# Optimization experiments

Hardware: AMD Instinct MI355X
Metric: run time of the kernel (lower is better)

Reference implementation:

```python
import jax, jax.numpy as jnp
import numpy as np

B, S, IN, H, SS = 128, 128, 2, 512, 100


def _gru_cell(x, h, Wi, Wh, bi, bh):
    # PyTorch GRU gate order: r, z, n
    gi = x @ Wi.T + bi
    gh = h @ Wh.T + bh
    ir, iz, inn = jnp.split(gi, 3, axis=-1)
    hr, hz, hn = jnp.split(gh, 3, axis=-1)
    r = jax.nn.sigmoid(ir + hr)
    z = jax.nn.sigmoid(iz + hz)
    n = jnp.tanh(inn + r * hn)
    return (1.0 - z) * n + z * h


def setup_inputs() -> dict:
    key = jax.random.key(0)
    ks = jax.random.split(key, 20)
    s = 1.0 / np.sqrt(H)
    inp = {
        "instance": jax.random.normal(ks[0], (B, S, IN), jnp.float32),
        "solution": jax.random.randint(ks[1], (B, S), 0, S),
        "instance_hidden": jax.random.normal(ks[2], (B, S, H), jnp.float32),
        "eps": jax.random.normal(ks[3], (B, SS), jnp.float32),
        # reference_embedding: Linear(IN -> H)
        "Wr": jax.random.normal(ks[4], (H, IN), jnp.float32) * s,
        "br": jnp.zeros((H,), jnp.float32),
        # rnn: GRU(H, H)
        "Wi1": jax.random.normal(ks[5], (3 * H, H), jnp.float32) * s,
        "Wh1": jax.random.normal(ks[6], (3 * H, H), jnp.float32) * s,
        "bi1": jnp.zeros((3 * H,), jnp.float32),
        "bh1": jnp.zeros((3 * H,), jnp.float32),
        # encoder_attn (additive)
        "Wa": jax.random.normal(ks[7], (H, H), jnp.float32) * s,
        "Ua": jax.random.normal(ks[8], (H, H), jnp.float32) * s,
        "v": jax.random.normal(ks[9], (H,), jnp.float32) * s,
        # gru_decoder: GRU(2H, H)
        "Wi2": jax.random.normal(ks[10], (3 * H, 2 * H), jnp.float32) * s,
        "Wh2": jax.random.normal(ks[11], (3 * H, H), jnp.float32) * s,
        "bi2": jnp.zeros((3 * H,), jnp.float32),
        "bh2": jnp.zeros((3 * H,), jnp.float32),
        # fc1 / fc2: Linear(H -> SS)
        "W1": jax.random.normal(ks[12], (SS, H), jnp.float32) * s,
        "b1": jnp.zeros((SS,), jnp.float32),
        "W2": jax.random.normal(ks[13], (SS, H), jnp.float32) * s,
        "b2": jnp.zeros((SS,), jnp.float32),
    }
    return inp


def reference(instance, solution, instance_hidden, eps, Wr, br, Wi1, Wh1, bi1, bh1,
              Wa, Ua, v, Wi2, Wh2, bi2, bh2, W1, b1, W2, b2):
    # gather reference nodes for every step, embed once: (B, L, H)
    inst_sel = jnp.take_along_axis(instance, solution[:, :, None], axis=1)  # (B,L,IN)
    ref_emb = inst_sel @ Wr.T + br                                          # (B,L,H)

    # precompute attention projection of the (static) instance encoding
    inst_proj = jnp.einsum("bsh,kh->bsk", instance_hidden, Wa)              # (B,S,H)

    L = solution.shape[1]
    x1_seq = jnp.swapaxes(ref_emb[:, : L - 1], 0, 1)  # (L-1,B,H) input to rnn (node j-1)
    x2_seq = jnp.swapaxes(ref_emb[:, 1:], 0, 1)       # (L-1,B,H) ref embed of node j

    def step(carry, xs):
        h1, h2 = carry
        x1, x2ref = xs
        h1 = _gru_cell(x1, h1, Wi1, Wh1, bi1, bh1)
        scores = jnp.einsum("bsh,h->bs", jnp.tanh(inst_proj + (h1 @ Ua.T)[:, None, :]), v)
        attn = jax.nn.softmax(scores, axis=-1)                 # (B,S)
        context = jnp.einsum("bs,bsh->bh", attn, instance_hidden)
        h2 = _gru_cell(jnp.concatenate([x2ref, context], axis=-1), h2, Wi2, Wh2, bi2, bh2)
        return (h1, h2), None

    h0 = jnp.zeros((instance.shape[0], Wh1.shape[1]), instance.dtype)
    (_, h2), _ = jax.lax.scan(step, (h0, h0), (x1_seq, x2_seq))

    mu = h2 @ W1.T + b1
    log_var = h2 @ W2.T + b2
    z = mu + eps * jnp.exp(0.5 * log_var)
    return z, mu, log_var
```

## Files before the change

kernel.cpp:

```cpp
#include <hip/hip_runtime.h>
#include <math.h>


__device__ __forceinline__ float sigm(float x){ return 1.0f/(1.0f+__expf(-x)); }
__device__ __forceinline__ float tanh_(float x){ float e=__expf(2.0f*x); return 1.0f-2.0f/(e+1.0f); }

__global__ __launch_bounds__(256)
void prep_kernel(const float* __restrict__ instance, const int* __restrict__ solution,
                 const float* __restrict__ Hst, const float* __restrict__ Wr,
                 const float* __restrict__ br, const float* __restrict__ Wi1,
                 const float* __restrict__ bi1, const float* __restrict__ Wh1,
                 const float* __restrict__ Wa, const float* __restrict__ Ua,
                 const float* __restrict__ Wi2, const float* __restrict__ Wh2,
                 const float* __restrict__ bi2,
                 float* __restrict__ P, float* __restrict__ WhT1, float* __restrict__ UaT,
                 float* __restrict__ WD, float* __restrict__ xselT,
                 float* __restrict__ A1f, float* __restrict__ A2f,
                 float* __restrict__ c1f, float* __restrict__ c2f,
                 float* __restrict__ h1T, float* __restrict__ vstack)
{
  const int w = blockIdx.x, t = threadIdx.x;
  __shared__ float smem[6656];

  if (w < 1024) {
    const int m0 = (w >> 3) * 128, h0 = (w & 7) * 64;
    const int hl = t & 15, mseg = t >> 4;
    float acc[4][8];
#pragma unroll
    for (int i = 0; i < 4; ++i)
#pragma unroll
      for (int r = 0; r < 8; ++r) acc[i][r] = 0.f;
    for (int kt = 0; kt < 16; ++kt) {
      {
        int row = t >> 1, cb = (t & 1) * 16;
        const float4* sp = (const float4*)(Hst + (size_t)(m0 + row) * 512 + kt * 32 + cb);
        float4 q0 = sp[0], q1 = sp[1], q2 = sp[2], q3 = sp[3];
        float vals[16] = {q0.x,q0.y,q0.z,q0.w,q1.x,q1.y,q1.z,q1.w,
                          q2.x,q2.y,q2.z,q2.w,q3.x,q3.y,q3.z,q3.w};
#pragma unroll
        for (int i = 0; i < 16; ++i) smem[(cb + i) * 136 + row] = vals[i];
      }
      {
        int row = t >> 2, cb = (t & 3) * 8;
        const float4* sp = (const float4*)(Wa + (size_t)(h0 + row) * 512 + kt * 32 + cb);
        float4 q0 = sp[0], q1 = sp[1];
        float vals[8] = {q0.x,q0.y,q0.z,q0.w,q1.x,q1.y,q1.z,q1.w};
#pragma unroll
        for (int i = 0; i < 8; ++i) smem[4352 + (cb + i) * 72 + row] = vals[i];
      }
      __syncthreads();
#pragma unroll 8
      for (int kk = 0; kk < 32; ++kk) {
        float4 wv = *(const float4*)&smem[4352 + kk * 72 + hl * 4];
        float4 ha = *(const float4*)&smem[kk * 136 + mseg * 8];
        float4 hb = *(const float4*)&smem[kk * 136 + mseg * 8 + 4];
        float wv_[4] = {wv.x, wv.y, wv.z, wv.w};
        float hv_[8] = {ha.x, ha.y, ha.z, ha.w, hb.x, hb.y, hb.z, hb.w};
#pragma unroll
        for (int i = 0; i < 4; ++i)
#pragma unroll
          for (int r = 0; r < 8; ++r) acc[i][r] += wv_[i] * hv_[r];
      }
      __syncthreads();
    }
#pragma unroll
    for (int r = 0; r < 8; ++r) {
      float4 st = {acc[0][r], acc[1][r], acc[2][r], acc[3][r]};
      *(float4*)&P[(size_t)(m0 + mseg * 8 + r) * 512 + h0 + hl * 4] = st;
    }

  } else if (w < 1664) {
    const int wt = w - 1024;
    const float* sp; float* dp; int r0, c0; size_t srs, drs;
    if (wt < 192)      { int q = wt;       sp = Wh1;       dp = WhT1;           r0=(q/8)*64; c0=(q%8)*64; srs=512;  drs=1536; }
    else if (wt < 384) { int q = wt - 192; sp = Wh2;       dp = WD;             r0=(q/8)*64; c0=(q%8)*64; srs=512;  drs=1536; }
    else if (wt < 576) { int q = wt - 384; sp = Wi2 + 512; dp = WD + 512*1536;  r0=(q/8)*64; c0=(q%8)*64; srs=1024; drs=1536; }
    else               { int q = wt - 576; sp = Ua;        dp = UaT;            r0=(q/8)*64; c0=(q%8)*64; srs=512;  drs=512;  }
    int row = t >> 2, cb = (t & 3) * 16;
    const float4* s2 = (const float4*)(sp + (size_t)(r0 + row) * srs + c0 + cb);
    float4 q0 = s2[0], q1 = s2[1], q2 = s2[2], q3 = s2[3];
    float vals[16] = {q0.x,q0.y,q0.z,q0.w,q1.x,q1.y,q1.z,q1.w,
                      q2.x,q2.y,q2.z,q2.w,q3.x,q3.y,q3.z,q3.w};
#pragma unroll
    for (int i = 0; i < 16; ++i) smem[row * 65 + cb + i] = vals[i];
    __syncthreads();
    float* d2 = dp + (size_t)(c0 + row) * drs + r0 + cb;
#pragma unroll
    for (int g = 0; g < 4; ++g) {
      float4 o = {smem[(cb + g*4 + 0) * 65 + row], smem[(cb + g*4 + 1) * 65 + row],
                  smem[(cb + g*4 + 2) * 65 + row], smem[(cb + g*4 + 3) * 65 + row]};
      *(float4*)(d2 + g * 4) = o;
    }

  } else if (w < 2048) {
    const int wf = w - 1664, wv = t >> 6, lane = t & 63;
    const int j = wf * 4 + wv;
    const float4* w1p = (const float4*)(Wi1 + (size_t)j * 512 + lane * 8);
    const float4* w2p = (const float4*)(Wi2 + (size_t)j * 1024 + lane * 8);
    const float4* wrp = (const float4*)(Wr + lane * 16);
    const float4* brp = (const float4*)(br + lane * 8);
    float4 u0 = w1p[0], u1 = w1p[1], v0 = w2p[0], v1 = w2p[1];
    float4 r0 = wrp[0], r1 = wrp[1], r2 = wrp[2], r3 = wrp[3];
    float4 bb0 = brp[0], bb1 = brp[1];
    float w1a[8] = {u0.x,u0.y,u0.z,u0.w,u1.x,u1.y,u1.z,u1.w};
    float w2a[8] = {v0.x,v0.y,v0.z,v0.w,v1.x,v1.y,v1.z,v1.w};
    float wr0[8] = {r0.x,r0.z,r1.x,r1.z,r2.x,r2.z,r3.x,r3.z};
    float wr1[8] = {r0.y,r0.w,r1.y,r1.w,r2.y,r2.w,r3.y,r3.w};
    float bra[8] = {bb0.x,bb0.y,bb0.z,bb0.w,bb1.x,bb1.y,bb1.z,bb1.w};
    float a0=0,a1=0,cc=0,b0=0,b1=0,cc2=0;
#pragma unroll
    for (int i = 0; i < 8; ++i) {
      a0 += w1a[i]*wr0[i]; a1 += w1a[i]*wr1[i]; cc  += w1a[i]*bra[i];
      b0 += w2a[i]*wr0[i]; b1 += w2a[i]*wr1[i]; cc2 += w2a[i]*bra[i];
    }
#pragma unroll
    for (int off = 32; off; off >>= 1) {
      a0 += __shfl_xor(a0, off); a1 += __shfl_xor(a1, off); cc  += __shfl_xor(cc, off);
      b0 += __shfl_xor(b0, off); b1 += __shfl_xor(b1, off); cc2 += __shfl_xor(cc2, off);
    }
    if (lane == 0) {
      A1f[j*2] = a0; A1f[j*2+1] = a1; c1f[j] = cc + bi1[j];
      A2f[j*2] = b0; A2f[j*2+1] = b1; c2f[j] = cc2 + bi2[j];
    }

  } else if (w == 2048) {
    for (int o = t; o < 32768; o += 256) {
      int b = o & 127, r = o >> 7, d = r & 1, l = r >> 1;
      int sel = solution[b * 128 + l];
      xselT[o] = instance[(size_t)(b * 128 + sel) * 2 + d];
    }
  } else {
    const int wz = w - 2049;
    for (int i = 0; i < 32; ++i) {
      int idx = wz * 8192 + i * 256 + t;
      h1T[65536 + idx] = 0.f;
      vstack[idx] = 0.f;
    }
  }
}

__global__ __launch_bounds__(512)
void step_kernel(int k, const float* __restrict__ Hst, const float* __restrict__ bh1,
                 const float* __restrict__ vvec, const float* __restrict__ bh2,
                 const float* __restrict__ P, const float* __restrict__ WhT1,
                 const float* __restrict__ UaT, const float* __restrict__ WD,
                 const float* __restrict__ xselT, const float* __restrict__ A1f,
                 const float* __restrict__ A2f, const float* __restrict__ c1f,
                 const float* __restrict__ c2f,
                 float* __restrict__ h1T, float* __restrict__ vstack,
                 float* __restrict__ uT, float* __restrict__ part,
                 float* __restrict__ mzbuf)
{
  const int w = blockIdx.x, t = threadIdx.x;
  __shared__ float lds[6144];

  if (w < 256) {
    const int tA = k; if (tA > 126) return;
    const int wv = __builtin_amdgcn_readfirstlane(t >> 6);
    const int lane = t & 63;
    const int c0 = w * 2;
    const float* h1p = h1T + ((tA + 1) & 1) * 65536;
    float acc[12];
#pragma unroll
    for (int i = 0; i < 12; ++i) acc[i] = 0.f;
    const float* hrow = h1p + wv * 64 * 128 + lane * 2;
    const float* wrow = WhT1 + (size_t)(wv * 64) * 1536 + c0;
    for (int kk = 0; kk < 64; ++kk) {
      float2 hv = *(const float2*)hrow;
      float w00 = wrow[0],    w01 = wrow[1];
      float w10 = wrow[512],  w11 = wrow[513];
      float w20 = wrow[1024], w21 = wrow[1025];
      acc[0] += hv.x*w00; acc[1] += hv.y*w00; acc[2]  += hv.x*w01; acc[3]  += hv.y*w01;
      acc[4] += hv.x*w10; acc[5] += hv.y*w10; acc[6]  += hv.x*w11; acc[7]  += hv.y*w11;
      acc[8] += hv.x*w20; acc[9] += hv.y*w20; acc[10] += hv.x*w21; acc[11] += hv.y*w21;
      hrow += 128; wrow += 1536;
    }
#pragma unroll
    for (int i = 0; i < 12; ++i) lds[(wv * 12 + i) * 64 + lane] = acc[i];
    __syncthreads();
    if (t < 256) {
      int b = t & 127, ci = t >> 7, ln = b >> 1, bs = b & 1;
      float gr = 0, gz = 0, gn = 0;
#pragma unroll
      for (int w2 = 0; w2 < 8; ++w2) {
        gr += lds[(w2 * 12 +     ci * 2 + bs) * 64 + ln];
        gz += lds[(w2 * 12 + 4 + ci * 2 + bs) * 64 + ln];
        gn += lds[(w2 * 12 + 8 + ci * 2 + bs) * 64 + ln];
      }
      int c = c0 + ci;
      float x0 = xselT[(tA * 2) * 128 + b], x1 = xselT[(tA * 2 + 1) * 128 + b];
      float ir  = A1f[c*2]*x0          + A1f[c*2+1]*x1          + c1f[c];
      float iz  = A1f[(c+512)*2]*x0    + A1f[(c+512)*2+1]*x1    + c1f[c+512];
      float in_ = A1f[(c+1024)*2]*x0   + A1f[(c+1024)*2+1]*x1   + c1f[c+1024];
      float r = sigm(ir + gr + bh1[c]);
      float z = sigm(iz + gz + bh1[c + 512]);
      float n = tanh_(in_ + r * (gn + bh1[c + 1024]));
      float hp = h1p[c * 128 + b];
      h1T[(tA & 1) * 65536 + c * 128 + b] = (1.f - z) * n + z * hp;
    }

  } else if (w < 384) {
    const int tU = k - 1; if (tU < 0 || tU > 126) return;
    const int wv = __builtin_amdgcn_readfirstlane(t >> 6);
    const int lane = t & 63;
    const int c0 = (w - 256) * 4;
    const float* h1c = h1T + (tU & 1) * 65536;
    float acc[8];
#pragma unroll
    for (int i = 0; i < 8; ++i) acc[i] = 0.f;
    const float* hrow = h1c + wv * 64 * 128 + lane * 2;
    const float* wrow = UaT + (size_t)(wv * 64) * 512 + c0;
    for (int kk = 0; kk < 64; ++kk) {
      float2 hv = *(const float2*)hrow;
      float w0 = wrow[0], w1 = wrow[1], w2 = wrow[2], w3 = wrow[3];
      acc[0] += hv.x*w0; acc[1] += hv.y*w0; acc[2] += hv.x*w1; acc[3] += hv.y*w1;
      acc[4] += hv.x*w2; acc[5] += hv.y*w2; acc[6] += hv.x*w3; acc[7] += hv.y*w3;
      hrow += 128; wrow += 512;
    }
#pragma unroll
    for (int i = 0; i < 8; ++i) lds[(wv * 8 + i) * 64 + lane] = acc[i];
    __syncthreads();
    {
      int b = t & 127, q = t >> 7;
      float u = 0;
#pragma unroll
      for (int w2 = 0; w2 < 8; ++w2) u += lds[(w2 * 8 + q * 2 + (b & 1)) * 64 + (b >> 1)];
      uT[(tU & 1) * 65536 + (c0 + q) * 128 + b] = u;
    }

  } else if (w < 896) {
    const int tB = k - 2; if (tB < 0 || tB > 126) return;
    const int wb = w - 384, b = wb >> 2, q = wb & 3;
    const int slot = tB & 1;
    float* uS = lds, *vS = lds + 512, *scS = lds + 1024, *wgt = lds + 1056;
    uS[t] = uT[slot * 65536 + t * 128 + b];
    vS[t] = vvec[t];
    __syncthreads();
    const int wv8 = t >> 6, lane = t & 63, h0 = lane * 8;
#pragma unroll
    for (int si = 0; si < 4; ++si) {
      int s = q * 32 + wv8 * 4 + si;
      const float* prow = P + (size_t)(b * 128 + s) * 512 + h0;
      float4 p0 = ((const float4*)prow)[0];
      float4 p1 = ((const float4*)prow)[1];
      float val = tanh_(p0.x + uS[h0+0]) * vS[h0+0]
                + tanh_(p0.y + uS[h0+1]) * vS[h0+1]
                + tanh_(p0.z + uS[h0+2]) * vS[h0+2]
                + tanh_(p0.w + uS[h0+3]) * vS[h0+3]
                + tanh_(p1.x + uS[h0+4]) * vS[h0+4]
                + tanh_(p1.y + uS[h0+5]) * vS[h0+5]
                + tanh_(p1.z + uS[h0+6]) * vS[h0+6]
                + tanh_(p1.w + uS[h0+7]) * vS[h0+7];
#pragma unroll
      for (int off = 32; off; off >>= 1) val += __shfl_xor(val, off);
      if (lane == 0) scS[wv8 * 4 + si] = val;
    }
    __syncthreads();
    if (t < 32) {
      float sc = scS[t], m = sc;
#pragma unroll
      for (int off = 16; off; off >>= 1) m = fmaxf(m, __shfl_xor(m, off));
      float e = __expf(sc - m);
      float zz = e;
#pragma unroll
      for (int off = 16; off; off >>= 1) zz += __shfl_xor(zz, off);
      wgt[t] = e;
      if (t == 0) {
        int mzi = ((slot * 4 + q) * 128 + b) * 2;
        mzbuf[mzi] = m; mzbuf[mzi + 1] = zz;
      }
    }
    __syncthreads();
    float a = 0.f;
    const float* hb = Hst + (size_t)(b * 128 + q * 32) * 512 + t;
#pragma unroll 8
    for (int s = 0; s < 32; ++s) a += wgt[s] * hb[(size_t)s * 512];
    part[((size_t)(slot * 4 + q) * 128 + b) * 512 + t] = a;

  } else if (w < 928) {
    const int tC = k - 3; if (tC < 0 || tC > 126) return;
    const int slot = tC & 1;
    float* scale = lds;
    if (t < 128) {
      int b = t;
      float m0 = mzbuf[((slot*4+0)*128+b)*2], z0 = mzbuf[((slot*4+0)*128+b)*2+1];
      float m1 = mzbuf[((slot*4+1)*128+b)*2], z1 = mzbuf[((slot*4+1)*128+b)*2+1];
      float m2 = mzbuf[((slot*4+2)*128+b)*2], z2 = mzbuf[((slot*4+2)*128+b)*2+1];
      float m3 = mzbuf[((slot*4+3)*128+b)*2], z3 = mzbuf[((slot*4+3)*128+b)*2+1];
      float M = fmaxf(fmaxf(m0, m1), fmaxf(m2, m3));
      float e0 = __expf(m0 - M), e1 = __expf(m1 - M), e2 = __expf(m2 - M), e3 = __expf(m3 - M);
      float inv = 1.f / (z0*e0 + z1*e1 + z2*e2 + z3*e3);
      scale[b] = e0*inv; scale[128+b] = e1*inv; scale[256+b] = e2*inv; scale[384+b] = e3*inv;
    }
    __syncthreads();
    const int base = (w - 896) * 2048;
#pragma unroll
    for (int i = 0; i < 4; ++i) {
      int o = base + i * 512 + t;
      int b = o & 127, kk = o >> 7;
      float vsum = scale[b]       * part[((size_t)(slot*4+0)*128 + b)*512 + kk]
                 + scale[128 + b] * part[((size_t)(slot*4+1)*128 + b)*512 + kk]
                 + scale[256 + b] * part[((size_t)(slot*4+2)*128 + b)*512 + kk]
                 + scale[384 + b] * part[((size_t)(slot*4+3)*128 + b)*512 + kk];
      vstack[slot * 131072 + (512 + kk) * 128 + b] = vsum;
    }

  } else {
    const int tD = k - 4; if (tD < 0 || tD > 126) return;
    const int wv = __builtin_amdgcn_readfirstlane(t >> 6);
    const int lane = t & 63;
    const int c0 = (w - 928) * 2;
    const int pair = tD & 1;
    const float* vs = vstack + pair * 131072;
    float acc[12];
#pragma unroll
    for (int i = 0; i < 12; ++i) acc[i] = 0.f;
    const float* hrow = vs + wv * 128 * 128 + lane * 2;
    const float* wrow = WD + (size_t)(wv * 128) * 1536 + c0;
    for (int kk = 0; kk < 128; ++kk) {
      float2 hv = *(const float2*)hrow;
      float w00 = wrow[0],    w01 = wrow[1];
      float w10 = wrow[512],  w11 = wrow[513];
      float w20 = wrow[1024], w21 = wrow[1025];
      acc[0] += hv.x*w00; acc[1] += hv.y*w00; acc[2]  += hv.x*w01; acc[3]  += hv.y*w01;
      acc[4] += hv.x*w10; acc[5] += hv.y*w10; acc[6]  += hv.x*w11; acc[7]  += hv.y*w11;
      acc[8] += hv.x*w20; acc[9] += hv.y*w20; acc[10] += hv.x*w21; acc[11] += hv.y*w21;
      hrow += 128; wrow += 1536;
    }
#pragma unroll
    for (int i = 0; i < 12; ++i) lds[(wv * 12 + i) * 64 + lane] = acc[i];
    __syncthreads();
    if (t < 256) {
      int b = t & 127, ci = t >> 7, ln = b >> 1, bs = b & 1;
      float gr = 0, gz = 0, gnh = 0, gni = 0;
#pragma unroll
      for (int w2 = 0; w2 < 8; ++w2) {
        gr += lds[(w2 * 12 +     ci * 2 + bs) * 64 + ln];
        gz += lds[(w2 * 12 + 4 + ci * 2 + bs) * 64 + ln];
        float g = lds[(w2 * 12 + 8 + ci * 2 + bs) * 64 + ln];
        if (w2 < 4) gnh += g; else gni += g;
      }
      int c = c0 + ci;
      float x0 = xselT[((tD + 1) * 2) * 128 + b], x1 = xselT[((tD + 1) * 2 + 1) * 128 + b];
      float ir  = A2f[c*2]*x0        + A2f[c*2+1]*x1        + c2f[c];
      float iz  = A2f[(c+512)*2]*x0  + A2f[(c+512)*2+1]*x1  + c2f[c+512];
      float in_ = A2f[(c+1024)*2]*x0 + A2f[(c+1024)*2+1]*x1 + c2f[c+1024] + gni;
      float r = sigm(ir + gr + bh2[c]);
      float z = sigm(iz + gz + bh2[c + 512]);
      float n = tanh_(in_ + r * (gnh + bh2[c + 1024]));
      float hp = vs[c * 128 + b];
      vstack[((tD + 1) & 1) * 131072 + c * 128 + b] = (1.f - z) * n + z * hp;
    }
  }
}

__global__ __launch_bounds__(128)
void final_kernel(const float* __restrict__ vstack, const float* __restrict__ eps,
                  const float* __restrict__ W1, const float* __restrict__ b1,
                  const float* __restrict__ W2, const float* __restrict__ b2,
                  float* __restrict__ out)
{
  const int b = blockIdx.x, t = threadIdx.x;
  __shared__ float hS[512];
  const float* h2 = vstack + 131072;
  for (int i = t; i < 512; i += 128) hS[i] = h2[i * 128 + b];
  __syncthreads();
  if (t < 100) {
    const float* w1 = W1 + (size_t)t * 512;
    const float* w2 = W2 + (size_t)t * 512;
    float mu = b1[t], lv = b2[t];
    for (int kk = 0; kk < 512; ++kk) { float h = hS[kk]; mu += h * w1[kk]; lv += h * w2[kk]; }
    float zz = mu + eps[b * 100 + t] * __expf(0.5f * lv);
    out[b * 100 + t] = zz;
    out[12800 + b * 100 + t] = mu;
    out[25600 + b * 100 + t] = lv;
  }
}

extern "C" void kernel_launch(void* const* d_in, const int* in_sizes, int n_in,
                              void* d_out, int out_size, void* d_ws, size_t ws_size,
                              hipStream_t stream)
{
  const float* instance = (const float*)d_in[0];
  const int*   solution = (const int*)d_in[1];
  const float* Hst      = (const float*)d_in[2];
  const float* eps      = (const float*)d_in[3];
  const float* Wr  = (const float*)d_in[4];
  const float* br  = (const float*)d_in[5];
  const float* Wi1 = (const float*)d_in[6];
  const float* Wh1 = (const float*)d_in[7];
  const float* bi1 = (const float*)d_in[8];
  const float* bh1 = (const float*)d_in[9];
  const float* Wa  = (const float*)d_in[10];
  const float* Ua  = (const float*)d_in[11];
  const float* v   = (const float*)d_in[12];
  const float* Wi2 = (const float*)d_in[13];
  const float* Wh2 = (const float*)d_in[14];
  const float* bi2 = (const float*)d_in[15];
  const float* bh2 = (const float*)d_in[16];
  const float* W1  = (const float*)d_in[17];
  const float* b1  = (const float*)d_in[18];
  const float* W2  = (const float*)d_in[19];
  const float* b2  = (const float*)d_in[20];

  float* wsf   = (float*)d_ws;
  float* P     = wsf;
  float* WhT1  = P     + 8388608;
  float* UaT   = WhT1  + 786432;
  float* WD    = UaT   + 262144;
  float* xselT = WD    + 1572864;
  float* A1f   = xselT + 32768;
  float* A2f   = A1f   + 3072;
  float* c1f   = A2f   + 3072;
  float* c2f   = c1f   + 1536;
  float* h1T   = c2f   + 1536;
  float* vstack= h1T   + 131072;
  float* uT    = vstack+ 262144;
  float* part  = uT    + 131072;
  float* mzbuf = part  + 524288;

  prep_kernel<<<dim3(2057), dim3(256), 0, stream>>>(
      instance, solution, Hst, Wr, br, Wi1, bi1, Wh1, Wa, Ua, Wi2, Wh2, bi2,
      P, WhT1, UaT, WD, xselT, A1f, A2f, c1f, c2f, h1T, vstack);

  for (int k = 0; k < 131; ++k)
    step_kernel<<<dim3(1184), dim3(512), 0, stream>>>(
        k, Hst, bh1, v, bh2, P, WhT1, UaT, WD, xselT, A1f, A2f, c1f, c2f,
        h1T, vstack, uT, part, mzbuf);

  final_kernel<<<dim3(128), dim3(128), 0, stream>>>(vstack, eps, W1, b1, W2, b2, (float*)d_out);
}
```

Before: 9.455 ms.

## Run GRU-attention recurrence in a persistent cooperative kernel with grid sync

```diff
diff --git a/kernel.cpp b/kernel.cpp
--- a/kernel.cpp
+++ b/kernel.cpp
@@ -1,5 +1,8 @@
 #include <hip/hip_runtime.h>
+#include <hip/hip_cooperative_groups.h>
 #include <math.h>
+
+namespace cg = cooperative_groups;
 
 
 __device__ __forceinline__ float sigm(float x){ return 1.0f/(1.0f+__expf(-x)); }
@@ -13,8 +16,8 @@
                  const float* __restrict__ Wa, const float* __restrict__ Ua,
                  const float* __restrict__ Wi2, const float* __restrict__ Wh2,
                  const float* __restrict__ bi2,
-                 float* __restrict__ P, float* __restrict__ WhT1, float* __restrict__ UaT,
-                 float* __restrict__ WD, float* __restrict__ xselT,
+                 float* __restrict__ P, float* __restrict__ WAs, float* __restrict__ WUs,
+                 float* __restrict__ WDs, float* __restrict__ xselT,
                  float* __restrict__ A1f, float* __restrict__ A2f,
                  float* __restrict__ c1f, float* __restrict__ c2f,
                  float* __restrict__ h1T, float* __restrict__ vstack)
@@ -31,23 +34,19 @@
 #pragma unroll
       for (int r = 0; r < 8; ++r) acc[i][r] = 0.f;
     for (int kt = 0; kt < 16; ++kt) {
-      {
-        int row = t >> 1, cb = (t & 1) * 16;
+      { int row = t >> 1, cb = (t & 1) * 16;
         const float4* sp = (const float4*)(Hst + (size_t)(m0 + row) * 512 + kt * 32 + cb);
         float4 q0 = sp[0], q1 = sp[1], q2 = sp[2], q3 = sp[3];
         float vals[16] = {q0.x,q0.y,q0.z,q0.w,q1.x,q1.y,q1.z,q1.w,
                           q2.x,q2.y,q2.z,q2.w,q3.x,q3.y,q3.z,q3.w};
 #pragma unroll
-        for (int i = 0; i < 16; ++i) smem[(cb + i) * 136 + row] = vals[i];
-      }
-      {
-        int row = t >> 2, cb = (t & 3) * 8;
+        for (int i = 0; i < 16; ++i) smem[(cb + i) * 136 + row] = vals[i]; }
+      { int row = t >> 2, cb = (t & 3) * 8;
         const float4* sp = (const float4*)(Wa + (size_t)(h0 + row) * 512 + kt * 32 + cb);
         float4 q0 = sp[0], q1 = sp[1];
         float vals[8] = {q0.x,q0.y,q0.z,q0.w,q1.x,q1.y,q1.z,q1.w};
 #pragma unroll
-        for (int i = 0; i < 8; ++i) smem[4352 + (cb + i) * 72 + row] = vals[i];
-      }
+        for (int i = 0; i < 8; ++i) smem[4352 + (cb + i) * 72 + row] = vals[i]; }
       __syncthreads();
 #pragma unroll 8
       for (int kk = 0; kk < 32; ++kk) {
@@ -69,29 +68,31 @@
       *(float4*)&P[(size_t)(m0 + mseg * 8 + r) * 512 + h0 + hl * 4] = st;
     }
 
+  } else if (w < 1216) {
+    for (int i = 0; i < 16; ++i) {
+      int e = (w - 1024) * 4096 + i * 256 + t;
+      int fc = e >> 9, k = e & 511;
+      int g = fc >> 9, c = fc & 511;
+      int wg = c >> 1, j = g * 2 + (c & 1);
+      WAs[((size_t)wg * 512 + k) * 8 + j] = Wh1[(size_t)fc * 512 + k];
+    }
+  } else if (w < 1280) {
+    for (int i = 0; i < 16; ++i) {
+      int e = (w - 1216) * 4096 + i * 256 + t;
+      int c = e >> 9, k = e & 511;
+      int wg = c >> 2, j = c & 3;
+      WUs[((size_t)wg * 512 + k) * 4 + j] = Ua[(size_t)c * 512 + k];
+    }
   } else if (w < 1664) {
-    const int wt = w - 1024;
-    const float* sp; float* dp; int r0, c0; size_t srs, drs;
-    if (wt < 192)      { int q = wt;       sp = Wh1;       dp = WhT1;           r0=(q/8)*64; c0=(q%8)*64; srs=512;  drs=1536; }
-    else if (wt < 384) { int q = wt - 192; sp = Wh2;       dp = WD;             r0=(q/8)*64; c0=(q%8)*64; srs=512;  drs=1536; }
-    else if (wt < 576) { int q = wt - 384; sp = Wi2 + 512; dp = WD + 512*1536;  r0=(q/8)*64; c0=(q%8)*64; srs=1024; drs=1536; }
-    else               { int q = wt - 576; sp = Ua;        dp = UaT;            r0=(q/8)*64; c0=(q%8)*64; srs=512;  drs=512;  }
-    int row = t >> 2, cb = (t & 3) * 16;
-    const float4* s2 = (const float4*)(sp + (size_t)(r0 + row) * srs + c0 + cb);
-    float4 q0 = s2[0], q1 = s2[1], q2 = s2[2], q3 = s2[3];
-    float vals[16] = {q0.x,q0.y,q0.z,q0.w,q1.x,q1.y,q1.z,q1.w,
-                      q2.x,q2.y,q2.z,q2.w,q3.x,q3.y,q3.z,q3.w};
-#pragma unroll
-    for (int i = 0; i < 16; ++i) smem[row * 65 + cb + i] = vals[i];
-    __syncthreads();
-    float* d2 = dp + (size_t)(c0 + row) * drs + r0 + cb;
-#pragma unroll
-    for (int g = 0; g < 4; ++g) {
-      float4 o = {smem[(cb + g*4 + 0) * 65 + row], smem[(cb + g*4 + 1) * 65 + row],
-                  smem[(cb + g*4 + 2) * 65 + row], smem[(cb + g*4 + 3) * 65 + row]};
-      *(float4*)(d2 + g * 4) = o;
-    }
-
+    for (int i = 0; i < 16; ++i) {
+      int e = (w - 1280) * 4096 + i * 256 + t;
+      int fc = e >> 10, k = e & 1023;
+      int g = fc >> 9, c = fc & 511;
+      int wg = c >> 1, j = g * 2 + (c & 1);
+      float src = (k < 512) ? Wh2[(size_t)fc * 512 + k]
+                            : Wi2[(size_t)fc * 1024 + 512 + (k - 512)];
+      WDs[((size_t)wg * 1024 + k) * 8 + j] = src;
+    }
   } else if (w < 2048) {
     const int wf = w - 1664, wv = t >> 6, lane = t & 63;
     const int j = wf * 4 + wv;
@@ -122,7 +123,6 @@
       A1f[j*2] = a0; A1f[j*2+1] = a1; c1f[j] = cc + bi1[j];
       A2f[j*2] = b0; A2f[j*2+1] = b1; c2f[j] = cc2 + bi2[j];
     }
-
   } else if (w == 2048) {
     for (int o = t; o < 32768; o += 256) {
       int b = o & 127, r = o >> 7, d = r & 1, l = r >> 1;
@@ -139,219 +139,242 @@
   }
 }
 
-__global__ __launch_bounds__(512)
-void step_kernel(int k, const float* __restrict__ Hst, const float* __restrict__ bh1,
-                 const float* __restrict__ vvec, const float* __restrict__ bh2,
-                 const float* __restrict__ P, const float* __restrict__ WhT1,
-                 const float* __restrict__ UaT, const float* __restrict__ WD,
-                 const float* __restrict__ xselT, const float* __restrict__ A1f,
-                 const float* __restrict__ A2f, const float* __restrict__ c1f,
-                 const float* __restrict__ c2f,
-                 float* __restrict__ h1T, float* __restrict__ vstack,
-                 float* __restrict__ uT, float* __restrict__ part,
-                 float* __restrict__ mzbuf)
-{
+__device__ __forceinline__ void round_body(
+    int k, int w, int t, int wv, int lane, float* lds,
+    const float* __restrict__ Hst, const float* __restrict__ bh1,
+    const float* __restrict__ vvec, const float* __restrict__ bh2,
+    const float* __restrict__ P, const float* __restrict__ WAs,
+    const float* __restrict__ WUs, const float* __restrict__ WDs,
+    const float* __restrict__ xselT, const float* __restrict__ A1f,
+    const float* __restrict__ A2f, const float* __restrict__ c1f,
+    const float* __restrict__ c2f,
+    float* __restrict__ h1T, float* __restrict__ vstack, float* __restrict__ uT)
+{
+  if (w < 256) {
+    const int tA = k;
+    if (tA <= 126) {
+      const int slotW = tA & 1, slotR = slotW ^ 1;
+      const float* hp = h1T + slotR * 65536 + (wv * 128) * 128 + lane * 2;
+      const float4* wp = (const float4*)(WAs + ((size_t)w * 512 + wv * 128) * 8);
+      float acc[12];
+#pragma unroll
+      for (int i = 0; i < 12; ++i) acc[i] = 0.f;
+#pragma unroll 4
+      for (int kk = 0; kk < 128; ++kk) {
+        float2 hv = *(const float2*)(hp + kk * 128);
+        float4 wa = wp[kk * 2], wb = wp[kk * 2 + 1];
+        acc[0] += hv.x*wa.x; acc[1]  += hv.y*wa.x;
+        acc[2] += hv.x*wa.y; acc[3]  += hv.y*wa.y;
+        acc[4] += hv.x*wa.z; acc[5]  += hv.y*wa.z;
+        acc[6] += hv.x*wa.w; acc[7]  += hv.y*wa.w;
+        acc[8] += hv.x*wb.x; acc[9]  += hv.y*wb.x;
+        acc[10]+= hv.x*wb.y; acc[11] += hv.y*wb.y;
+      }
+#pragma unroll
+      for (int i = 0; i < 12; ++i) lds[wv * 768 + i * 64 + lane] = acc[i];
+      __syncthreads();
+      { int b = t & 127, ci = t >> 7, l = b >> 1, bs = b & 1;
+        float gr = 0, gz = 0, gn = 0;
+#pragma unroll
+        for (int w2 = 0; w2 < 4; ++w2) {
+          gr += lds[w2 * 768 + (    ci * 2 + bs) * 64 + l];
+          gz += lds[w2 * 768 + (4 + ci * 2 + bs) * 64 + l];
+          gn += lds[w2 * 768 + (8 + ci * 2 + bs) * 64 + l];
+        }
+        int c = w * 2 + ci;
+        float x0 = xselT[(tA * 2) * 128 + b], x1 = xselT[(tA * 2 + 1) * 128 + b];
+        float ir  = A1f[c*2]*x0        + A1f[c*2+1]*x1        + c1f[c];
+        float iz  = A1f[(c+512)*2]*x0  + A1f[(c+512)*2+1]*x1  + c1f[c+512];
+        float in_ = A1f[(c+1024)*2]*x0 + A1f[(c+1024)*2+1]*x1 + c1f[c+1024];
+        float r = sigm(ir + gr + bh1[c]);
+        float z = sigm(iz + gz + bh1[c + 512]);
+        float n = tanh_(in_ + r * (gn + bh1[c + 1024]));
+        float hpv = h1T[slotR * 65536 + c * 128 + b];
+        h1T[slotW * 65536 + c * 128 + b] = (1.f - z) * n + z * hpv;
+      }
+      __syncthreads();
+    }
+  } else if (w < 384) {
+    const int tU = k - 1;
+    if (tU >= 0 && tU <= 126) {
+      const int slot = tU & 1;
+      const float* hp = h1T + slot * 65536 + (wv * 128) * 128 + lane * 2;
+      const float4* wp = (const float4*)(WUs + ((size_t)(w - 256) * 512 + wv * 128) * 4);
+      float acc[8];
+#pragma unroll
+      for (int i = 0; i < 8; ++i) acc[i] = 0.f;
+#pragma unroll 4
+      for (int kk = 0; kk < 128; ++kk) {
+        float2 hv = *(const float2*)(hp + kk * 128);
+        float4 wq = wp[kk];
+        acc[0] += hv.x*wq.x; acc[1] += hv.y*wq.x;
+        acc[2] += hv.x*wq.y; acc[3] += hv.y*wq.y;
+        acc[4] += hv.x*wq.z; acc[5] += hv.y*wq.z;
+        acc[6] += hv.x*wq.w; acc[7] += hv.y*wq.w;
+      }
+#pragma unroll
+      for (int i = 0; i < 8; ++i) lds[wv * 512 + i * 64 + lane] = acc[i];
+      __syncthreads();
+      { int b = t & 127, qq = t >> 7, l = b >> 1, bs = b & 1;
+        int c0 = (w - 256) * 4;
+#pragma unroll
+        for (int jj = 0; jj < 2; ++jj) {
+          int j = qq + jj * 2;
+          float u = 0;
+#pragma unroll
+          for (int w2 = 0; w2 < 4; ++w2) u += lds[w2 * 512 + (j * 2 + bs) * 64 + l];
+          uT[slot * 65536 + (c0 + j) * 128 + b] = u;
+        }
+      }
+      __syncthreads();
+    }
+  } else if (w < 512) {
+    const int tB = k - 2;
+    if (tB >= 0 && tB <= 126) {
+      const int b = w - 384, slot = tB & 1;
+      float* uS = lds; float* vS = lds + 512; float* scS = lds + 1024; float* wS = lds + 1152;
+      uS[t]       = uT[slot * 65536 + t * 128 + b];
+      uS[t + 256] = uT[slot * 65536 + (t + 256) * 128 + b];
+      vS[t] = vvec[t]; vS[t + 256] = vvec[t + 256];
+      __syncthreads();
+      const int h0 = lane * 8;
+#pragma unroll 2
+      for (int si = 0; si < 32; ++si) {
+        int s = wv * 32 + si;
+        const float* prow = P + ((size_t)(b * 128 + s)) * 512 + h0;
+        float4 p0 = ((const float4*)prow)[0];
+        float4 p1 = ((const float4*)prow)[1];
+        float val = tanh_(p0.x + uS[h0+0]) * vS[h0+0]
+                  + tanh_(p0.y + uS[h0+1]) * vS[h0+1]
+                  + tanh_(p0.z + uS[h0+2]) * vS[h0+2]
+                  + tanh_(p0.w + uS[h0+3]) * vS[h0+3]
+                  + tanh_(p1.x + uS[h0+4]) * vS[h0+4]
+                  + tanh_(p1.y + uS[h0+5]) * vS[h0+5]
+                  + tanh_(p1.z + uS[h0+6]) * vS[h0+6]
+                  + tanh_(p1.w + uS[h0+7]) * vS[h0+7];
+#pragma unroll
+        for (int off = 32; off; off >>= 1) val += __shfl_xor(val, off);
+        if (lane == 0) scS[s] = val;
+      }
+      __syncthreads();
+      if (t < 64) {
+        float sc0 = scS[t], sc1 = scS[t + 64];
+        float m = fmaxf(sc0, sc1);
+#pragma unroll
+        for (int off = 32; off; off >>= 1) m = fmaxf(m, __shfl_xor(m, off));
+        float e0 = __expf(sc0 - m), e1 = __expf(sc1 - m);
+        float zz = e0 + e1;
+#pragma unroll
+        for (int off = 32; off; off >>= 1) zz += __shfl_xor(zz, off);
+        float inv = 1.f / zz;
+        wS[t] = e0 * inv; wS[t + 64] = e1 * inv;
+      }
+      __syncthreads();
+      { float acc0 = 0.f, acc1 = 0.f;
+        const float* hb = Hst + (size_t)(b * 128) * 512;
+#pragma unroll 8
+        for (int s = 0; s < 128; ++s) {
+          float ws_ = wS[s];
+          acc0 += ws_ * hb[(size_t)s * 512 + t];
+          acc1 += ws_ * hb[(size_t)s * 512 + t + 256];
+        }
+        vstack[slot * 131072 + (512 + t) * 128 + b] = acc0;
+        vstack[slot * 131072 + (512 + t + 256) * 128 + b] = acc1;
+      }
+      __syncthreads();
+    }
+  } else {
+    const int tD = k - 3;
+    if (tD >= 0 && tD <= 126) {
+      const int wd = w - 512, slot = tD & 1, nslot = slot ^ 1;
+      const float* vsp = vstack + slot * 131072;
+      const float* hp = vsp + (wv * 256) * 128 + lane * 2;
+      const float4* wp = (const float4*)(WDs + ((size_t)wd * 1024 + wv * 256) * 8);
+      float acc[12];
+#pragma unroll
+      for (int i = 0; i < 12; ++i) acc[i] = 0.f;
+#pragma unroll 4
+      for (int kk = 0; kk < 256; ++kk) {
+        float2 hv = *(const float2*)(hp + kk * 128);
+        float4 wa = wp[kk * 2], wb = wp[kk * 2 + 1];
+        acc[0] += hv.x*wa.x; acc[1]  += hv.y*wa.x;
+        acc[2] += hv.x*wa.y; acc[3]  += hv.y*wa.y;
+        acc[4] += hv.x*wa.z; acc[5]  += hv.y*wa.z;
+        acc[6] += hv.x*wa.w; acc[7]  += hv.y*wa.w;
+        acc[8] += hv.x*wb.x; acc[9]  += hv.y*wb.x;
+        acc[10]+= hv.x*wb.y; acc[11] += hv.y*wb.y;
+      }
+#pragma unroll
+      for (int i = 0; i < 12; ++i) lds[wv * 768 + i * 64 + lane] = acc[i];
+      __syncthreads();
+      { int b = t & 127, ci = t >> 7, l = b >> 1, bs = b & 1;
+        float gr = 0, gz = 0, gnh = 0, gni = 0;
+#pragma unroll
+        for (int w2 = 0; w2 < 4; ++w2) {
+          gr += lds[w2 * 768 + (    ci * 2 + bs) * 64 + l];
+          gz += lds[w2 * 768 + (4 + ci * 2 + bs) * 64 + l];
+          float g = lds[w2 * 768 + (8 + ci * 2 + bs) * 64 + l];
+          if (w2 < 2) gnh += g; else gni += g;
+        }
+        int c = wd * 2 + ci;
+        float x0 = xselT[((tD + 1) * 2) * 128 + b], x1 = xselT[((tD + 1) * 2 + 1) * 128 + b];
+        float ir  = A2f[c*2]*x0        + A2f[c*2+1]*x1        + c2f[c];
+        float iz  = A2f[(c+512)*2]*x0  + A2f[(c+512)*2+1]*x1  + c2f[c+512];
+        float in_ = A2f[(c+1024)*2]*x0 + A2f[(c+1024)*2+1]*x1 + c2f[c+1024] + gni;
+        float r = sigm(ir + gr + bh2[c]);
+        float z = sigm(iz + gz + bh2[c + 512]);
+        float n = tanh_(in_ + r * (gnh + bh2[c + 1024]));
+        float hpv = vsp[c * 128 + b];
+        vstack[nslot * 131072 + c * 128 + b] = (1.f - z) * n + z * hpv;
+      }
+      __syncthreads();
+    }
+  }
+}
+
+__global__ void __launch_bounds__(256, 3)
+persist_kernel(const float* __restrict__ Hst, const float* __restrict__ bh1,
+               const float* __restrict__ vvec, const float* __restrict__ bh2,
+               const float* __restrict__ P, const float* __restrict__ WAs,
+               const float* __restrict__ WUs, const float* __restrict__ WDs,
+               const float* __restrict__ xselT, const float* __restrict__ A1f,
+               const float* __restrict__ A2f, const float* __restrict__ c1f,
+               const float* __restrict__ c2f,
+               float* __restrict__ h1T, float* __restrict__ vstack,
+               float* __restrict__ uT)
+{
+  cg::grid_group grid = cg::this_grid();
   const int w = blockIdx.x, t = threadIdx.x;
-  __shared__ float lds[6144];
-
-  if (w < 256) {
-    const int tA = k; if (tA > 126) return;
-    const int wv = __builtin_amdgcn_readfirstlane(t >> 6);
-    const int lane = t & 63;
-    const int c0 = w * 2;
-    const float* h1p = h1T + ((tA + 1) & 1) * 65536;
-    float acc[12];
-#pragma unroll
-    for (int i = 0; i < 12; ++i) acc[i] = 0.f;
-    const float* hrow = h1p + wv * 64 * 128 + lane * 2;
-    const float* wrow = WhT1 + (size_t)(wv * 64) * 1536 + c0;
-    for (int kk = 0; kk < 64; ++kk) {
-      float2 hv = *(const float2*)hrow;
-      float w00 = wrow[0],    w01 = wrow[1];
-      float w10 = wrow[512],  w11 = wrow[513];
-      float w20 = wrow[1024], w21 = wrow[1025];
-      acc[0] += hv.x*w00; acc[1] += hv.y*w00; acc[2]  += hv.x*w01; acc[3]  += hv.y*w01;
-      acc[4] += hv.x*w10; acc[5] += hv.y*w10; acc[6]  += hv.x*w11; acc[7]  += hv.y*w11;
-      acc[8] += hv.x*w20; acc[9] += hv.y*w20; acc[10] += hv.x*w21; acc[11] += hv.y*w21;
-      hrow += 128; wrow += 1536;
-    }
-#pragma unroll
-    for (int i = 0; i < 12; ++i) lds[(wv * 12 + i) * 64 + lane] = acc[i];
-    __syncthreads();
-    if (t < 256) {
-      int b = t & 127, ci = t >> 7, ln = b >> 1, bs = b & 1;
-      float gr = 0, gz = 0, gn = 0;
-#pragma unroll
-      for (int w2 = 0; w2 < 8; ++w2) {
-        gr += lds[(w2 * 12 +     ci * 2 + bs) * 64 + ln];
-        gz += lds[(w2 * 12 + 4 + ci * 2 + bs) * 64 + ln];
-        gn += lds[(w2 * 12 + 8 + ci * 2 + bs) * 64 + ln];
-      }
-      int c = c0 + ci;
-      float x0 = xselT[(tA * 2) * 128 + b], x1 = xselT[(tA * 2 + 1) * 128 + b];
-      float ir  = A1f[c*2]*x0          + A1f[c*2+1]*x1          + c1f[c];
-      float iz  = A1f[(c+512)*2]*x0    + A1f[(c+512)*2+1]*x1    + c1f[c+512];
-      float in_ = A1f[(c+1024)*2]*x0   + A1f[(c+1024)*2+1]*x1   + c1f[c+1024];
-      float r = sigm(ir + gr + bh1[c]);
-      float z = sigm(iz + gz + bh1[c + 512]);
-      float n = tanh_(in_ + r * (gn + bh1[c + 1024]));
-      float hp = h1p[c * 128 + b];
-      h1T[(tA & 1) * 65536 + c * 128 + b] = (1.f - z) * n + z * hp;
-    }
-
-  } else if (w < 384) {
-    const int tU = k - 1; if (tU < 0 || tU > 126) return;
-    const int wv = __builtin_amdgcn_readfirstlane(t >> 6);
-    const int lane = t & 63;
-    const int c0 = (w - 256) * 4;
-    const float* h1c = h1T + (tU & 1) * 65536;
-    float acc[8];
-#pragma unroll
-    for (int i = 0; i < 8; ++i) acc[i] = 0.f;
-    const float* hrow = h1c + wv * 64 * 128 + lane * 2;
-    const float* wrow = UaT + (size_t)(wv * 64) * 512 + c0;
-    for (int kk = 0; kk < 64; ++kk) {
-      float2 hv = *(const float2*)hrow;
-      float w0 = wrow[0], w1 = wrow[1], w2 = wrow[2], w3 = wrow[3];
-      acc[0] += hv.x*w0; acc[1] += hv.y*w0; acc[2] += hv.x*w1; acc[3] += hv.y*w1;
-      acc[4] += hv.x*w2; acc[5] += hv.y*w2; acc[6] += hv.x*w3; acc[7] += hv.y*w3;
-      hrow += 128; wrow += 512;
-    }
-#pragma unroll
-    for (int i = 0; i < 8; ++i) lds[(wv * 8 + i) * 64 + lane] = acc[i];
-    __syncthreads();
-    {
-      int b = t & 127, q = t >> 7;
-      float u = 0;
-#pragma unroll
-      for (int w2 = 0; w2 < 8; ++w2) u += lds[(w2 * 8 + q * 2 + (b & 1)) * 64 + (b >> 1)];
-      uT[(tU & 1) * 65536 + (c0 + q) * 128 + b] = u;
-    }
-
-  } else if (w < 896) {
-    const int tB = k - 2; if (tB < 0 || tB > 126) return;
-    const int wb = w - 384, b = wb >> 2, q = wb & 3;
-    const int slot = tB & 1;
-    float* uS = lds, *vS = lds + 512, *scS = lds + 1024, *wgt = lds + 1056;
-    uS[t] = uT[slot * 65536 + t * 128 + b];
-    vS[t] = vvec[t];
-    __syncthreads();
-    const int wv8 = t >> 6, lane = t & 63, h0 = lane * 8;
-#pragma unroll
-    for (int si = 0; si < 4; ++si) {
-      int s = q * 32 + wv8 * 4 + si;
-      const float* prow = P + (size_t)(b * 128 + s) * 512 + h0;
-      float4 p0 = ((const float4*)prow)[0];
-      float4 p1 = ((const float4*)prow)[1];
-      float val = tanh_(p0.x + uS[h0+0]) * vS[h0+0]
-                + tanh_(p0.y + uS[h0+1]) * vS[h0+1]
-                + tanh_(p0.z + uS[h0+2]) * vS[h0+2]
-                + tanh_(p0.w + uS[h0+3]) * vS[h0+3]
-                + tanh_(p1.x + uS[h0+4]) * vS[h0+4]
-                + tanh_(p1.y + uS[h0+5]) * vS[h0+5]
-                + tanh_(p1.z + uS[h0+6]) * vS[h0+6]
-                + tanh_(p1.w + uS[h0+7]) * vS[h0+7];
-#pragma unroll
-      for (int off = 32; off; off >>= 1) val += __shfl_xor(val, off);
-      if (lane == 0) scS[wv8 * 4 + si] = val;
-    }
-    __syncthreads();
-    if (t < 32) {
-      float sc = scS[t], m = sc;
-#pragma unroll
-      for (int off = 16; off; off >>= 1) m = fmaxf(m, __shfl_xor(m, off));
-      float e = __expf(sc - m);
-      float zz = e;
-#pragma unroll
-      for (int off = 16; off; off >>= 1) zz += __shfl_xor(zz, off);
-      wgt[t] = e;
-      if (t == 0) {
-        int mzi = ((slot * 4 + q) * 128 + b) * 2;
-        mzbuf[mzi] = m; mzbuf[mzi + 1] = zz;
-      }
-    }
-    __syncthreads();
-    float a = 0.f;
-    const float* hb = Hst + (size_t)(b * 128 + q * 32) * 512 + t;
-#pragma unroll 8
-    for (int s = 0; s < 32; ++s) a += wgt[s] * hb[(size_t)s * 512];
-    part[((size_t)(slot * 4 + q) * 128 + b) * 512 + t] = a;
-
-  } else if (w < 928) {
-    const int tC = k - 3; if (tC < 0 || tC > 126) return;
-    const int slot = tC & 1;
-    float* scale = lds;
-    if (t < 128) {
-      int b = t;
-      float m0 = mzbuf[((slot*4+0)*128+b)*2], z0 = mzbuf[((slot*4+0)*128+b)*2+1];
-      float m1 = mzbuf[((slot*4+1)*128+b)*2], z1 = mzbuf[((slot*4+1)*128+b)*2+1];
-      float m2 = mzbuf[((slot*4+2)*128+b)*2], z2 = mzbuf[((slot*4+2)*128+b)*2+1];
-      float m3 = mzbuf[((slot*4+3)*128+b)*2], z3 = mzbuf[((slot*4+3)*128+b)*2+1];
-      float M = fmaxf(fmaxf(m0, m1), fmaxf(m2, m3));
-      float e0 = __expf(m0 - M), e1 = __expf(m1 - M), e2 = __expf(m2 - M), e3 = __expf(m3 - M);
-      float inv = 1.f / (z0*e0 + z1*e1 + z2*e2 + z3*e3);
-      scale[b] = e0*inv; scale[128+b] = e1*inv; scale[256+b] = e2*inv; scale[384+b] = e3*inv;
-    }
-    __syncthreads();
-    const int base = (w - 896) * 2048;
-#pragma unroll
-    for (int i = 0; i < 4; ++i) {
-      int o = base + i * 512 + t;
-      int b = o & 127, kk = o >> 7;
-      float vsum = scale[b]       * part[((size_t)(slot*4+0)*128 + b)*512 + kk]
-                 + scale[128 + b] * part[((size_t)(slot*4+1)*128 + b)*512 + kk]
-                 + scale[256 + b] * part[((size_t)(slot*4+2)*128 + b)*512 + kk]
-                 + scale[384 + b] * part[((size_t)(slot*4+3)*128 + b)*512 + kk];
-      vstack[slot * 131072 + (512 + kk) * 128 + b] = vsum;
-    }
-
-  } else {
-    const int tD = k - 4; if (tD < 0 || tD > 126) return;
-    const int wv = __builtin_amdgcn_readfirstlane(t >> 6);
-    const int lane = t & 63;
-    const int c0 = (w - 928) * 2;
-    const int pair = tD & 1;
-    const float* vs = vstack + pair * 131072;
-    float acc[12];
-#pragma unroll
-    for (int i = 0; i < 12; ++i) acc[i] = 0.f;
-    const float* hrow = vs + wv * 128 * 128 + lane * 2;
-    const float* wrow = WD + (size_t)(wv * 128) * 1536 + c0;
-    for (int kk = 0; kk < 128; ++kk) {
-      float2 hv = *(const float2*)hrow;
-      float w00 = wrow[0],    w01 = wrow[1];
-      float w10 = wrow[512],  w11 = wrow[513];
-      float w20 = wrow[1024], w21 = wrow[1025];
-      acc[0] += hv.x*w00; acc[1] += hv.y*w00; acc[2]  += hv.x*w01; acc[3]  += hv.y*w01;
-      acc[4] += hv.x*w10; acc[5] += hv.y*w10; acc[6]  += hv.x*w11; acc[7]  += hv.y*w11;
-      acc[8] += hv.x*w20; acc[9] += hv.y*w20; acc[10] += hv.x*w21; acc[11] += hv.y*w21;
-      hrow += 128; wrow += 1536;
-    }
-#pragma unroll
-    for (int i = 0; i < 12; ++i) lds[(wv * 12 + i) * 64 + lane] = acc[i];
-    __syncthreads();
-    if (t < 256) {
-      int b = t & 127, ci = t >> 7, ln = b >> 1, bs = b & 1;
-      float gr = 0, gz = 0, gnh = 0, gni = 0;
-#pragma unroll
-      for (int w2 = 0; w2 < 8; ++w2) {
-        gr += lds[(w2 * 12 +     ci * 2 + bs) * 64 + ln];
-        gz += lds[(w2 * 12 + 4 + ci * 2 + bs) * 64 + ln];
-        float g = lds[(w2 * 12 + 8 + ci * 2 + bs) * 64 + ln];
-        if (w2 < 4) gnh += g; else gni += g;
-      }
-      int c = c0 + ci;
-      float x0 = xselT[((tD + 1) * 2) * 128 + b], x1 = xselT[((tD + 1) * 2 + 1) * 128 + b];
-      float ir  = A2f[c*2]*x0        + A2f[c*2+1]*x1        + c2f[c];
-      float iz  = A2f[(c+512)*2]*x0  + A2f[(c+512)*2+1]*x1  + c2f[c+512];
-      float in_ = A2f[(c+1024)*2]*x0 + A2f[(c+1024)*2+1]*x1 + c2f[c+1024] + gni;
-      float r = sigm(ir + gr + bh2[c]);
-      float z = sigm(iz + gz + bh2[c + 512]);
-      float n = tanh_(in_ + r * (gnh + bh2[c + 1024]));
-      float hp = vs[c * 128 + b];
-      vstack[((tD + 1) & 1) * 131072 + c * 128 + b] = (1.f - z) * n + z * hp;
-    }
+  const int wv = __builtin_amdgcn_readfirstlane(t >> 6);
+  const int lane = t & 63;
+  __shared__ float lds[3072];
+
+  for (int k = 0; k < 130; ++k) {
+    round_body(k, w, t, wv, lane, lds, Hst, bh1, vvec, bh2, P, WAs, WUs, WDs,
+               xselT, A1f, A2f, c1f, c2f, h1T, vstack, uT);
+    __threadfence();
+    grid.sync();
+    __threadfence();
   }
+}
+
+__global__ void __launch_bounds__(256, 3)
+round_kernel(int k, const float* __restrict__ Hst, const float* __restrict__ bh1,
+             const float* __restrict__ vvec, const float* __restrict__ bh2,
+             const float* __restrict__ P, const float* __restrict__ WAs,
+             const float* __restrict__ WUs, const float* __restrict__ WDs,
+             const float* __restrict__ xselT, const float* __restrict__ A1f,
+             const float* __restrict__ A2f, const float* __restrict__ c1f,
+             const float* __restrict__ c2f,
+             float* __restrict__ h1T, float* __restrict__ vstack,
+             float* __restrict__ uT)
+{
+  const int w = blockIdx.x, t = threadIdx.x;
+  const int wv = __builtin_amdgcn_readfirstlane(t >> 6);
+  const int lane = t & 63;
+  __shared__ float lds[3072];
+  round_body(k, w, t, wv, lane, lds, Hst, bh1, vvec, bh2, P, WAs, WUs, WDs,
+             xselT, A1f, A2f, c1f, c2f, h1T, vstack, uT);
 }
 
 __global__ __launch_bounds__(128)
@@ -405,10 +428,10 @@
 
   float* wsf   = (float*)d_ws;
   float* P     = wsf;
-  float* WhT1  = P     + 8388608;
-  float* UaT   = WhT1  + 786432;
-  float* WD    = UaT   + 262144;
-  float* xselT = WD    + 1572864;
+  float* WAs   = P     + 8388608;
+  float* WUs   = WAs   + 1048576;
+  float* WDs   = WUs   + 262144;
+  float* xselT = WDs   + 2097152;
   float* A1f   = xselT + 32768;
   float* A2f   = A1f   + 3072;
   float* c1f   = A2f   + 3072;
@@ -416,17 +439,27 @@
   float* h1T   = c2f   + 1536;
   float* vstack= h1T   + 131072;
   float* uT    = vstack+ 262144;
-  float* part  = uT    + 131072;
-  float* mzbuf = part  + 524288;
 
   prep_kernel<<<dim3(2057), dim3(256), 0, stream>>>(
       instance, solution, Hst, Wr, br, Wi1, bi1, Wh1, Wa, Ua, Wi2, Wh2, bi2,
-      P, WhT1, UaT, WD, xselT, A1f, A2f, c1f, c2f, h1T, vstack);
-
-  for (int k = 0; k < 131; ++k)
-    step_kernel<<<dim3(1184), dim3(512), 0, stream>>>(
-        k, Hst, bh1, v, bh2, P, WhT1, UaT, WD, xselT, A1f, A2f, c1f, c2f,
-        h1T, vstack, uT, part, mzbuf);
+      P, WAs, WUs, WDs, xselT, A1f, A2f, c1f, c2f, h1T, vstack);
+
+  const float *Hst_ = Hst, *bh1_ = bh1, *v_ = v, *bh2_ = bh2;
+  const float *P_ = P, *WAs_ = WAs, *WUs_ = WUs, *WDs_ = WDs;
+  const float *xselT_ = xselT, *A1f_ = A1f, *A2f_ = A2f, *c1f_ = c1f, *c2f_ = c2f;
+  float *h1T_ = h1T, *vstack_ = vstack, *uT_ = uT;
+  void* args[] = {(void*)&Hst_, (void*)&bh1_, (void*)&v_, (void*)&bh2_,
+                  (void*)&P_, (void*)&WAs_, (void*)&WUs_, (void*)&WDs_,
+                  (void*)&xselT_, (void*)&A1f_, (void*)&A2f_, (void*)&c1f_,
+                  (void*)&c2f_, (void*)&h1T_, (void*)&vstack_, (void*)&uT_};
+  hipError_t rc = hipLaunchCooperativeKernel((void*)persist_kernel, dim3(768),
+                                             dim3(256), args, 0, stream);
+  if (rc != hipSuccess) {
+    for (int k = 0; k < 130; ++k)
+      round_kernel<<<dim3(768), dim3(256), 0, stream>>>(
+          k, Hst, bh1, v, bh2, P, WAs, WUs, WDs, xselT, A1f, A2f, c1f, c2f,
+          h1T, vstack, uT);
+  }
 
   final_kernel<<<dim3(128), dim3(128), 0, stream>>>(vstack, eps, W1, b1, W2, b2, (float*)d_out);
 }
```

Result: slower. 33.03 ms (+249.4%).
